# Optimization experiments

Measured on AMD Instinct MI355X. Metric: run time of the kernel, lower is better.

The kernel has to match this reference:

```python
import jax, jax.numpy as jnp
import numpy as np

N, E = 500000, 128
H1, H2, H3, OUT = 256, 128, 64, 1
IN = 3 * E


def setup_inputs() -> dict:
    key = jax.random.key(0)
    ks = jax.random.split(key, 12)
    s = 0.02
    return {
        "encoder": jax.random.normal(ks[0], (N, E), dtype=jnp.float32),
        "current_state_tsr": jax.random.randint(ks[1], (N, 1), 0, 2, dtype=jnp.int32),
        "W1": jax.random.normal(ks[2], (IN, H1), dtype=jnp.float32) * s,
        "b1": jnp.zeros((H1,), dtype=jnp.float32),
        "W2": jax.random.normal(ks[3], (H1, H2), dtype=jnp.float32) * s,
        "b2": jnp.zeros((H2,), dtype=jnp.float32),
        "W3": jax.random.normal(ks[4], (H2, H3), dtype=jnp.float32) * s,
        "b3": jnp.zeros((H3,), dtype=jnp.float32),
        "W4": jax.random.normal(ks[5], (H3, OUT), dtype=jnp.float32) * s,
        "b4": jnp.zeros((OUT,), dtype=jnp.float32),
        "graph": 1,
    }


def reference(encoder, current_state_tsr, W1, b1, W2, b2, W3, b3, W4, b4, graph):
    n = encoder.shape[0]
    cs = current_state_tsr  # [N,1] int state flags
    # masked node features (zeros where mask fails), then single-graph max readout
    in_state = jnp.where(cs > 0, encoder, 0.0)            # [N,E]
    mu_in = jax.nn.relu(jnp.max(in_state, axis=0, keepdims=True))   # [1,E]
    not_in_state = jnp.where(cs == 0, encoder, 0.0)       # [N,E]
    mu_not = jax.nn.relu(jnp.max(not_in_state, axis=0, keepdims=True))  # [1,E]
    feats = jnp.concatenate(
        [jnp.broadcast_to(mu_in, (n, mu_in.shape[1])),
         jnp.broadcast_to(mu_not, (n, mu_not.shape[1])),
         encoder], axis=1)                                # [N,3E]
    h = jax.nn.leaky_relu(feats @ W1 + b1)
    h = jax.nn.leaky_relu(h @ W2 + b2)
    h = jax.nn.leaky_relu(h @ W3 + b3)
    logits = h @ W4 + b4                                  # [N,1]
    q = jax.nn.softmax(logits, axis=0)                    # softmax across nodes
    return q.squeeze(axis=1)                              # [N]
```

## Files before the change

### kernel.cpp

```cpp
#include <hip/hip_runtime.h>
#include <hip/hip_bf16.h>

#define NN 500000
#define NBLK_CM 2000

typedef unsigned short ushort_t;
typedef __attribute__((ext_vector_type(8))) __bf16 bf16x8;
typedef __attribute__((ext_vector_type(2))) __bf16 bf16x2;
typedef __attribute__((ext_vector_type(4))) float f32x4;
typedef __attribute__((ext_vector_type(4))) unsigned uint4v;

__device__ inline ushort_t f2bf(float f) {
  unsigned u = __builtin_bit_cast(unsigned, f);
  return (ushort_t)((u + 0x7FFFu + ((u >> 16) & 1u)) >> 16);
}
__device__ inline float lrelu(float v) { return fmaxf(v, 0.f) + 0.01f * fminf(v, 0.f); }
__device__ inline unsigned pk2(float lo, float hi) {
  bf16x2 v; v[0] = (__bf16)lo; v[1] = (__bf16)hi;
  return __builtin_bit_cast(unsigned, v);
}
__device__ inline bf16x8 mk8(unsigned w0, unsigned w1, unsigned w2, unsigned w3) {
  uint4v u; u.x = w0; u.y = w1; u.z = w2; u.w = w3;
  return __builtin_bit_cast(bf16x8, u);
}
#define SHF(v, s) ((unsigned)__shfl((int)(v), (s), 64))
#define SBAR() __builtin_amdgcn_sched_barrier(0)

__global__ __launch_bounds__(256) void k_colmax(
    const float* __restrict__ enc, const int* __restrict__ cs,
    float* __restrict__ partials)
{
  __shared__ float4 s_in[256], s_not[256];
  const int tid = threadIdx.x;
  const int c4 = tid & 31;
  const int rs = tid >> 5;
  const long base = (long)blockIdx.x * 250;
  float4 mi = {0.f, 0.f, 0.f, 0.f}, mn = {0.f, 0.f, 0.f, 0.f};
  const float4* e4 = (const float4*)enc;
  #pragma unroll 4
  for (int it = 0; it < 32; ++it) {
    long r = base + rs + 8L * it;
    if (r < base + 250 && r < NN) {
      float4 v = e4[r * 32 + c4];
      bool ins = cs[r] > 0;
      mi.x = fmaxf(mi.x, ins ? v.x : 0.f); mi.y = fmaxf(mi.y, ins ? v.y : 0.f);
      mi.z = fmaxf(mi.z, ins ? v.z : 0.f); mi.w = fmaxf(mi.w, ins ? v.w : 0.f);
      mn.x = fmaxf(mn.x, ins ? 0.f : v.x); mn.y = fmaxf(mn.y, ins ? 0.f : v.y);
      mn.z = fmaxf(mn.z, ins ? 0.f : v.z); mn.w = fmaxf(mn.w, ins ? 0.f : v.w);
    }
  }
  s_in[tid] = mi; s_not[tid] = mn;
  __syncthreads();
  if (tid < 32) {
    for (int j = 1; j < 8; ++j) {
      float4 a = s_in[j * 32 + tid], b = s_not[j * 32 + tid];
      mi.x = fmaxf(mi.x, a.x); mi.y = fmaxf(mi.y, a.y);
      mi.z = fmaxf(mi.z, a.z); mi.w = fmaxf(mi.w, a.w);
      mn.x = fmaxf(mn.x, b.x); mn.y = fmaxf(mn.y, b.y);
      mn.z = fmaxf(mn.z, b.z); mn.w = fmaxf(mn.w, b.w);
    }
    float* po = partials + (size_t)blockIdx.x * 256;
    ((float4*)po)[tid] = mi;
    ((float4*)(po + 128))[tid] = mn;
  }
}

__global__ __launch_bounds__(256) void k_red1(
    const float* __restrict__ partials, float* __restrict__ red2)
{
  const int tid = threadIdx.x, b = blockIdx.x;
  float m = 0.f;
  #pragma unroll 8
  for (int row = b; row < NBLK_CM; row += 64)
    m = fmaxf(m, partials[(size_t)row * 256 + tid]);
  red2[b * 256 + tid] = m;
}

__global__ __launch_bounds__(1024) void k_red2(
    const float* __restrict__ red2,
    float* __restrict__ mu_in, float* __restrict__ mu_not)
{
  __shared__ float sT[1024];
  const int tid = threadIdx.x;
  const int col = tid & 255, sl = tid >> 8;
  float m = 0.f;
  #pragma unroll
  for (int j = 0; j < 16; ++j)
    m = fmaxf(m, red2[(sl * 16 + j) * 256 + col]);
  sT[tid] = m;
  __syncthreads();
  if (tid < 256) {
    m = fmaxf(fmaxf(sT[tid], sT[tid + 256]), fmaxf(sT[tid + 512], sT[tid + 768]));
    if (tid < 128) mu_in[tid] = m;
    else           mu_not[tid - 128] = m;
  }
}

__global__ __launch_bounds__(512)
__attribute__((amdgpu_waves_per_eu(2, 2)))
void k_mlp(
    const float* __restrict__ enc,
    const float* __restrict__ W1, const float* __restrict__ b1,
    const float* __restrict__ W2, const float* __restrict__ b2,
    const float* __restrict__ W3, const float* __restrict__ b3,
    const float* __restrict__ W4, const float* __restrict__ b4,
    const float* __restrict__ mu_in, const float* __restrict__ mu_not,
    float* __restrict__ eL, float* __restrict__ psum)
{
  __shared__ ushort_t sW1[256 * 136];
  __shared__ ushort_t sW2[128 * 264];
  __shared__ ushort_t sW3[64 * 136];
  __shared__ float sC[520];
  __shared__ float sT[512];

  const int tid = threadIdx.x;

  for (int idx = tid; idx < 32768; idx += 512) {
    int n = idx & 255, k = idx >> 8;
    sW1[n * 136 + k] = f2bf(W1[(256 + k) * 256 + n]);
  }
  for (int idx = tid; idx < 32768; idx += 512) {
    int n = idx & 127, k = idx >> 7;
    sW2[n * 264 + k] = f2bf(W2[k * 128 + n]);
  }
  for (int idx = tid; idx < 8192; idx += 512) {
    int n = idx & 63, k = idx >> 6;
    sW3[n * 136 + k] = f2bf(W3[k * 64 + n]);
  }
  if (tid >= 256 && tid < 384) sC[tid] = b2[tid - 256];
  else if (tid >= 384 && tid < 448) sC[tid] = b3[tid - 384];
  else if (tid >= 448) sC[tid] = W4[tid - 448];
  if (tid == 0) sC[512] = b4[0];
  {
    const int j = tid & 255, h = tid >> 8;
    float c = h ? 0.f : b1[j];
    #pragma unroll 8
    for (int e = 64 * h; e < 64 * h + 64; ++e) {
      c += mu_in[e]  * W1[e * 256 + j];
      c += mu_not[e] * W1[(128 + e) * 256 + j];
    }
    sT[tid] = c;
  }
  __syncthreads();
  if (tid < 256) sC[tid] = sT[tid] + sT[tid + 256];
  __syncthreads();

  const int wave = tid >> 6, lane = tid & 63;
  const int lr = lane & 15, lg = lane >> 4;
  const int wid = blockIdx.x * 8 + wave;
  const int selhi = lane & 32;
  const int srcLo = lr + ((lane & 16) << 1);
  const int srcHi = srcLo + 16;

  const ushort_t* w1p = sW1 + lr * 136 + 8 * lg;
  const ushort_t* w2p = sW2 + lr * 264 + 8 * lg;
  const ushort_t* w3p = sW3 + lr * 136 + 8 * lg;

  float es = 0.f;
  bf16x8 B1[4];

  {
    const float4* p = (const float4*)(enc + (size_t)(wid * 16 + lr) * 128);
    #pragma unroll
    for (int kt = 0; kt < 4; ++kt) {
      float4 f0 = p[kt * 8 + lg * 2], f1 = p[kt * 8 + lg * 2 + 1];
      bf16x8 a;
      a[0] = (__bf16)f0.x; a[1] = (__bf16)f0.y; a[2] = (__bf16)f0.z; a[3] = (__bf16)f0.w;
      a[4] = (__bf16)f1.x; a[5] = (__bf16)f1.y; a[6] = (__bf16)f1.z; a[7] = (__bf16)f1.w;
      B1[kt] = a;
    }
  }

  for (int r0 = wid * 16; r0 < NN; r0 += 32768) {
    bf16x8 B2[8];
    #pragma unroll
    for (int p = 0; p < 8; ++p) {
      f32x4 a0 = (f32x4){0.f, 0.f, 0.f, 0.f}, a1 = (f32x4){0.f, 0.f, 0.f, 0.f};
      #pragma unroll
      for (int kt = 0; kt < 4; ++kt) {
        bf16x8 wA = *(const bf16x8*)(w1p + (2 * p) * 2176 + kt * 32);
        bf16x8 wB = *(const bf16x8*)(w1p + (2 * p + 1) * 2176 + kt * 32);
        a0 = __builtin_amdgcn_mfma_f32_16x16x32_bf16(wA, B1[kt], a0, 0, 0, 0);
        a1 = __builtin_amdgcn_mfma_f32_16x16x32_bf16(wB, B1[kt], a1, 0, 0, 0);
      }
      float4 cb0 = *(const float4*)(sC + 16 * (2 * p) + 4 * lg);
      float4 cb1 = *(const float4*)(sC + 16 * (2 * p + 1) + 4 * lg);
      unsigned q0 = pk2(lrelu(a0[0] + cb0.x), lrelu(a0[1] + cb0.y));
      unsigned q1 = pk2(lrelu(a0[2] + cb0.z), lrelu(a0[3] + cb0.w));
      unsigned q2 = pk2(lrelu(a1[0] + cb1.x), lrelu(a1[1] + cb1.y));
      unsigned q3 = pk2(lrelu(a1[2] + cb1.z), lrelu(a1[3] + cb1.w));
      unsigned w0a = SHF(q0, srcLo), w0b = SHF(q2, srcLo);
      unsigned w1a = SHF(q1, srcLo), w1b = SHF(q3, srcLo);
      unsigned w2a = SHF(q0, srcHi), w2b = SHF(q2, srcHi);
      unsigned w3a = SHF(q1, srcHi), w3b = SHF(q3, srcHi);
      B2[p] = mk8(selhi ? w0b : w0a, selhi ? w1b : w1a,
                  selhi ? w2b : w2a, selhi ? w3b : w3a);
    }
    SBAR();
    bf16x8 B3[4];
    #pragma unroll
    for (int p = 0; p < 4; ++p) {
      f32x4 a0 = (f32x4){0.f, 0.f, 0.f, 0.f}, a1 = (f32x4){0.f, 0.f, 0.f, 0.f};
      #pragma unroll
      for (int kt = 0; kt < 8; ++kt) {
        bf16x8 wA = *(const bf16x8*)(w2p + (2 * p) * 4224 + kt * 32);
        bf16x8 wB = *(const bf16x8*)(w2p + (2 * p + 1) * 4224 + kt * 32);
        a0 = __builtin_amdgcn_mfma_f32_16x16x32_bf16(wA, B2[kt], a0, 0, 0, 0);
        a1 = __builtin_amdgcn_mfma_f32_16x16x32_bf16(wB, B2[kt], a1, 0, 0, 0);
      }
      float4 cb0 = *(const float4*)(sC + 256 + 16 * (2 * p) + 4 * lg);
      float4 cb1 = *(const float4*)(sC + 256 + 16 * (2 * p + 1) + 4 * lg);
      unsigned q0 = pk2(lrelu(a0[0] + cb0.x), lrelu(a0[1] + cb0.y));
      unsigned q1 = pk2(lrelu(a0[2] + cb0.z), lrelu(a0[3] + cb0.w));
      unsigned q2 = pk2(lrelu(a1[0] + cb1.x), lrelu(a1[1] + cb1.y));
      unsigned q3 = pk2(lrelu(a1[2] + cb1.z), lrelu(a1[3] + cb1.w));
      unsigned w0a = SHF(q0, srcLo), w0b = SHF(q2, srcLo);
      unsigned w1a = SHF(q1, srcLo), w1b = SHF(q3, srcLo);
      unsigned w2a = SHF(q0, srcHi), w2b = SHF(q2, srcHi);
      unsigned w3a = SHF(q1, srcHi), w3b = SHF(q3, srcHi);
      B3[p] = mk8(selhi ? w0b : w0a, selhi ? w1b : w1a,
                  selhi ? w2b : w2a, selhi ? w3b : w3a);
    }
    SBAR();
    int rn = r0 + 32768; if (rn >= NN) rn = r0;
    float4 tA[8];
    {
      const float4* p = (const float4*)(enc + (size_t)(rn + lr) * 128);
      #pragma unroll
      for (int kt = 0; kt < 4; ++kt) {
        tA[2 * kt]     = p[kt * 8 + lg * 2];
        tA[2 * kt + 1] = p[kt * 8 + lg * 2 + 1];
      }
    }
    SBAR();
    float dot = 0.f;
    #pragma unroll
    for (int p = 0; p < 2; ++p) {
      f32x4 a0 = (f32x4){0.f, 0.f, 0.f, 0.f}, a1 = (f32x4){0.f, 0.f, 0.f, 0.f};
      #pragma unroll
      for (int kt = 0; kt < 4; ++kt) {
        bf16x8 wA = *(const bf16x8*)(w3p + (2 * p) * 2176 + kt * 32);
        bf16x8 wB = *(const bf16x8*)(w3p + (2 * p + 1) * 2176 + kt * 32);
        a0 = __builtin_amdgcn_mfma_f32_16x16x32_bf16(wA, B3[kt], a0, 0, 0, 0);
        a1 = __builtin_amdgcn_mfma_f32_16x16x32_bf16(wB, B3[kt], a1, 0, 0, 0);
      }
      float4 cb0  = *(const float4*)(sC + 384 + 16 * (2 * p) + 4 * lg);
      float4 cb1  = *(const float4*)(sC + 384 + 16 * (2 * p + 1) + 4 * lg);
      float4 w4v0 = *(const float4*)(sC + 448 + 16 * (2 * p) + 4 * lg);
      float4 w4v1 = *(const float4*)(sC + 448 + 16 * (2 * p + 1) + 4 * lg);
      dot += lrelu(a0[0] + cb0.x) * w4v0.x + lrelu(a0[1] + cb0.y) * w4v0.y
           + lrelu(a0[2] + cb0.z) * w4v0.z + lrelu(a0[3] + cb0.w) * w4v0.w;
      dot += lrelu(a1[0] + cb1.x) * w4v1.x + lrelu(a1[1] + cb1.y) * w4v1.y
           + lrelu(a1[2] + cb1.z) * w4v1.z + lrelu(a1[3] + cb1.w) * w4v1.w;
    }
    dot += __shfl_xor(dot, 16, 64);
    dot += __shfl_xor(dot, 32, 64);
    float ev = expf(dot + sC[512]);
    if (lg == 0) eL[r0 + lr] = ev;
    es += ev;
    #pragma unroll
    for (int kt = 0; kt < 4; ++kt) {
      float4 f0 = tA[2 * kt], f1 = tA[2 * kt + 1];
      bf16x8 a;
      a[0] = (__bf16)f0.x; a[1] = (__bf16)f0.y; a[2] = (__bf16)f0.z; a[3] = (__bf16)f0.w;
      a[4] = (__bf16)f1.x; a[5] = (__bf16)f1.y; a[6] = (__bf16)f1.z; a[7] = (__bf16)f1.w;
      B1[kt] = a;
    }
  }
  #pragma unroll
  for (int off = 1; off < 64; off <<= 1) es += __shfl_xor(es, off, 64);
  if (lane == 0) psum[wid] = 0.25f * es;
}

__global__ __launch_bounds__(256) void k_finalsum(const float* __restrict__ psum,
                                                  float* __restrict__ scal)
{
  const int tid = threadIdx.x;
  float s = 0.f;
  #pragma unroll
  for (int k = 0; k < 8; ++k) s += psum[tid + k * 256];
  #pragma unroll
  for (int off = 1; off < 64; off <<= 1) s += __shfl_xor(s, off, 64);
  __shared__ float sr[4];
  if ((tid & 63) == 0) sr[tid >> 6] = s;
  __syncthreads();
  if (tid == 0) scal[0] = 1.f / (sr[0] + sr[1] + sr[2] + sr[3]);
}

__global__ __launch_bounds__(256) void k_norm(const float* __restrict__ eL,
                                              const float* __restrict__ scal,
                                              float* __restrict__ out)
{
  const float inv = scal[0];
  const int i = blockIdx.x * 256 + threadIdx.x;
  if (i < NN / 4) {
    float4 v = ((const float4*)eL)[i];
    float4 o = {v.x * inv, v.y * inv, v.z * inv, v.w * inv};
    ((float4*)out)[i] = o;
  }
}

extern "C" void kernel_launch(void* const* d_in, const int* in_sizes, int n_in,
                              void* d_out, int out_size, void* d_ws, size_t ws_size,
                              hipStream_t stream) {
  const float* enc = (const float*)d_in[0];
  const int*   cs  = (const int*)d_in[1];
  const float* W1  = (const float*)d_in[2];
  const float* b1  = (const float*)d_in[3];
  const float* W2  = (const float*)d_in[4];
  const float* b2  = (const float*)d_in[5];
  const float* W3  = (const float*)d_in[6];
  const float* b3  = (const float*)d_in[7];
  const float* W4  = (const float*)d_in[8];
  const float* b4  = (const float*)d_in[9];
  float* out = (float*)d_out;

  char* ws = (char*)d_ws;
  float* mu_in  = (float*)(ws + 0);
  float* mu_not = (float*)(ws + 512);
  float* psum   = (float*)(ws + 2048);
  float* scal   = (float*)(ws + 10240);
  float* red2   = (float*)(ws + 16384);
  float* eLbuf  = (float*)(ws + 131072);
  float* partials = (float*)(ws + 131072);

  k_colmax<<<dim3(NBLK_CM), dim3(256), 0, stream>>>(enc, cs, partials);
  k_red1<<<dim3(64), dim3(256), 0, stream>>>(partials, red2);
  k_red2<<<dim3(1), dim3(1024), 0, stream>>>(red2, mu_in, mu_not);
  k_mlp<<<dim3(256), dim3(512), 0, stream>>>(enc, W1, b1, W2, b2, W3, b3, W4, b4,
                                             mu_in, mu_not, eLbuf, psum);
  k_finalsum<<<dim3(1), dim3(256), 0, stream>>>(psum, scal);
  k_norm<<<dim3(489), dim3(256), 0, stream>>>(eLbuf, scal, out);
}
```

Measured before the change: 192.7 us.

## XOR-swizzle bf16 weight tiles in LDS and use butterfly xor-shuffles

Drops the padded row strides for the bf16 weight tiles in shared memory and replaces them with an unpadded layout whose 8-element chunk index is rotated per row, so the MFMA A-operand reads stay free of bank conflicts while using less LDS. The 8 indexed shuffles per layer that rebuild the B operand for the next layer become a two-stage butterfly with 4 xor shuffles plus selects. Both aim to cut LDS and cross-lane traffic in the inner MLP loop. The risk is added address arithmetic and a mistake in the swizzle or butterfly mapping.

New measurement: 182.9 us. -5.1%, faster.

```diff
diff --git a/kernel.cpp b/kernel.cpp
--- a/kernel.cpp
+++ b/kernel.cpp
@@ -23,8 +23,22 @@
   uint4v u; u.x = w0; u.y = w1; u.z = w2; u.w = w3;
   return __builtin_bit_cast(bf16x8, u);
 }
-#define SHF(v, s) ((unsigned)__shfl((int)(v), (s), 64))
+#define SHF_X(v, m) ((unsigned)__shfl_xor((int)(v), (m), 64))
 #define SBAR() __builtin_amdgcn_sched_barrier(0)
+
+__device__ inline void bfly4(unsigned q0, unsigned q1, unsigned q2, unsigned q3,
+                             bool b0, bool b1,
+                             unsigned& w0, unsigned& w1, unsigned& w2, unsigned& w3)
+{
+  unsigned vA0 = b1 ? q0 : q2, vA1 = b1 ? q1 : q3;
+  unsigned eA0 = SHF_X(vA0, 32), eA1 = SHF_X(vA1, 32);
+  unsigned s00 = b1 ? eA0 : q0, s01 = b1 ? eA1 : q1;
+  unsigned s10 = b1 ? q2 : eA0, s11 = b1 ? q3 : eA1;
+  unsigned vB0 = b0 ? s00 : s10, vB1 = b0 ? s01 : s11;
+  unsigned eB0 = SHF_X(vB0, 16), eB1 = SHF_X(vB1, 16);
+  w0 = b0 ? eB0 : s00; w1 = b0 ? eB1 : s01;
+  w2 = b0 ? s10 : eB0; w3 = b0 ? s11 : eB1;
+}
 
 __global__ __launch_bounds__(256) void k_colmax(
     const float* __restrict__ enc, const int* __restrict__ cs,
@@ -107,9 +121,9 @@
     const float* __restrict__ mu_in, const float* __restrict__ mu_not,
     float* __restrict__ eL, float* __restrict__ psum)
 {
-  __shared__ ushort_t sW1[256 * 136];
-  __shared__ ushort_t sW2[128 * 264];
-  __shared__ ushort_t sW3[64 * 136];
+  __shared__ ushort_t sW1[256 * 128];
+  __shared__ ushort_t sW2[128 * 256];
+  __shared__ ushort_t sW3[64 * 128];
   __shared__ float sC[520];
   __shared__ float sT[512];
 
@@ -117,15 +131,18 @@
 
   for (int idx = tid; idx < 32768; idx += 512) {
     int n = idx & 255, k = idx >> 8;
-    sW1[n * 136 + k] = f2bf(W1[(256 + k) * 256 + n]);
+    int bp = ((k >> 3) + 2 * n) & 15;
+    sW1[n * 128 + bp * 8 + (k & 7)] = f2bf(W1[(256 + k) * 256 + n]);
   }
   for (int idx = tid; idx < 32768; idx += 512) {
     int n = idx & 127, k = idx >> 7;
-    sW2[n * 264 + k] = f2bf(W2[k * 128 + n]);
+    int bp = ((k >> 3) + 2 * n) & 31;
+    sW2[n * 256 + bp * 8 + (k & 7)] = f2bf(W2[k * 128 + n]);
   }
   for (int idx = tid; idx < 8192; idx += 512) {
     int n = idx & 63, k = idx >> 6;
-    sW3[n * 136 + k] = f2bf(W3[k * 64 + n]);
+    int bp = ((k >> 3) + 2 * n) & 15;
+    sW3[n * 128 + bp * 8 + (k & 7)] = f2bf(W3[k * 64 + n]);
   }
   if (tid >= 256 && tid < 384) sC[tid] = b2[tid - 256];
   else if (tid >= 384 && tid < 448) sC[tid] = b3[tid - 384];
@@ -148,13 +165,12 @@
   const int wave = tid >> 6, lane = tid & 63;
   const int lr = lane & 15, lg = lane >> 4;
   const int wid = blockIdx.x * 8 + wave;
-  const int selhi = lane & 32;
-  const int srcLo = lr + ((lane & 16) << 1);
-  const int srcHi = srcLo + 16;
-
-  const ushort_t* w1p = sW1 + lr * 136 + 8 * lg;
-  const ushort_t* w2p = sW2 + lr * 264 + 8 * lg;
-  const ushort_t* w3p = sW3 + lr * 136 + 8 * lg;
+  const bool b0 = lg & 1, b1f = lg & 2;
+  const int sw = lg + 2 * lr;
+
+  const ushort_t* w1p = sW1 + lr * 128;
+  const ushort_t* w2p = sW2 + lr * 256;
+  const ushort_t* w3p = sW3 + lr * 128;
 
   float es = 0.f;
   bf16x8 B1[4];
@@ -178,8 +194,8 @@
       f32x4 a0 = (f32x4){0.f, 0.f, 0.f, 0.f}, a1 = (f32x4){0.f, 0.f, 0.f, 0.f};
       #pragma unroll
       for (int kt = 0; kt < 4; ++kt) {
-        bf16x8 wA = *(const bf16x8*)(w1p + (2 * p) * 2176 + kt * 32);
-        bf16x8 wB = *(const bf16x8*)(w1p + (2 * p + 1) * 2176 + kt * 32);
+        bf16x8 wA = *(const bf16x8*)(w1p + (2 * p) * 2048 + (((4 * kt + sw) & 15) << 3));
+        bf16x8 wB = *(const bf16x8*)(w1p + (2 * p + 1) * 2048 + (((4 * kt + sw) & 15) << 3));
         a0 = __builtin_amdgcn_mfma_f32_16x16x32_bf16(wA, B1[kt], a0, 0, 0, 0);
         a1 = __builtin_amdgcn_mfma_f32_16x16x32_bf16(wB, B1[kt], a1, 0, 0, 0);
       }
@@ -189,12 +205,9 @@
       unsigned q1 = pk2(lrelu(a0[2] + cb0.z), lrelu(a0[3] + cb0.w));
       unsigned q2 = pk2(lrelu(a1[0] + cb1.x), lrelu(a1[1] + cb1.y));
       unsigned q3 = pk2(lrelu(a1[2] + cb1.z), lrelu(a1[3] + cb1.w));
-      unsigned w0a = SHF(q0, srcLo), w0b = SHF(q2, srcLo);
-      unsigned w1a = SHF(q1, srcLo), w1b = SHF(q3, srcLo);
-      unsigned w2a = SHF(q0, srcHi), w2b = SHF(q2, srcHi);
-      unsigned w3a = SHF(q1, srcHi), w3b = SHF(q3, srcHi);
-      B2[p] = mk8(selhi ? w0b : w0a, selhi ? w1b : w1a,
-                  selhi ? w2b : w2a, selhi ? w3b : w3a);
+      unsigned w0, w1, w2, w3;
+      bfly4(q0, q1, q2, q3, b0, b1f, w0, w1, w2, w3);
+      B2[p] = mk8(w0, w1, w2, w3);
     }
     SBAR();
     bf16x8 B3[4];
@@ -203,8 +216,8 @@
       f32x4 a0 = (f32x4){0.f, 0.f, 0.f, 0.f}, a1 = (f32x4){0.f, 0.f, 0.f, 0.f};
       #pragma unroll
       for (int kt = 0; kt < 8; ++kt) {
-        bf16x8 wA = *(const bf16x8*)(w2p + (2 * p) * 4224 + kt * 32);
-        bf16x8 wB = *(const bf16x8*)(w2p + (2 * p + 1) * 4224 + kt * 32);
+        bf16x8 wA = *(const bf16x8*)(w2p + (2 * p) * 4096 + (((4 * kt + sw) & 31) << 3));
+        bf16x8 wB = *(const bf16x8*)(w2p + (2 * p + 1) * 4096 + (((4 * kt + sw) & 31) << 3));
         a0 = __builtin_amdgcn_mfma_f32_16x16x32_bf16(wA, B2[kt], a0, 0, 0, 0);
         a1 = __builtin_amdgcn_mfma_f32_16x16x32_bf16(wB, B2[kt], a1, 0, 0, 0);
       }
@@ -214,12 +227,9 @@
       unsigned q1 = pk2(lrelu(a0[2] + cb0.z), lrelu(a0[3] + cb0.w));
       unsigned q2 = pk2(lrelu(a1[0] + cb1.x), lrelu(a1[1] + cb1.y));
       unsigned q3 = pk2(lrelu(a1[2] + cb1.z), lrelu(a1[3] + cb1.w));
-      unsigned w0a = SHF(q0, srcLo), w0b = SHF(q2, srcLo);
-      unsigned w1a = SHF(q1, srcLo), w1b = SHF(q3, srcLo);
-      unsigned w2a = SHF(q0, srcHi), w2b = SHF(q2, srcHi);
-      unsigned w3a = SHF(q1, srcHi), w3b = SHF(q3, srcHi);
-      B3[p] = mk8(selhi ? w0b : w0a, selhi ? w1b : w1a,
-                  selhi ? w2b : w2a, selhi ? w3b : w3a);
+      unsigned w0, w1, w2, w3;
+      bfly4(q0, q1, q2, q3, b0, b1f, w0, w1, w2, w3);
+      B3[p] = mk8(w0, w1, w2, w3);
     }
     SBAR();
     int rn = r0 + 32768; if (rn >= NN) rn = r0;
@@ -239,8 +249,8 @@
       f32x4 a0 = (f32x4){0.f, 0.f, 0.f, 0.f}, a1 = (f32x4){0.f, 0.f, 0.f, 0.f};
       #pragma unroll
       for (int kt = 0; kt < 4; ++kt) {
-        bf16x8 wA = *(const bf16x8*)(w3p + (2 * p) * 2176 + kt * 32);
-        bf16x8 wB = *(const bf16x8*)(w3p + (2 * p + 1) * 2176 + kt * 32);
+        bf16x8 wA = *(const bf16x8*)(w3p + (2 * p) * 2048 + (((4 * kt + sw) & 15) << 3));
+        bf16x8 wB = *(const bf16x8*)(w3p + (2 * p + 1) * 2048 + (((4 * kt + sw) & 15) << 3));
         a0 = __builtin_amdgcn_mfma_f32_16x16x32_bf16(wA, B3[kt], a0, 0, 0, 0);
         a1 = __builtin_amdgcn_mfma_f32_16x16x32_bf16(wB, B3[kt], a1, 0, 0, 0);
       }
```
